# Optimization experiments

Hardware: AMD Instinct MI355X
Metric: run time of the kernel (lower is better)

## Reference

```python
import jax, jax.numpy as jnp
import numpy as np

B, S, D, H = 4, 2048, 1024, 16
HD = D // H

def setup_inputs() -> dict:
    key = jax.random.key(0)
    ks = jax.random.split(key, 11)
    s = 1.0 / np.sqrt(D)
    return {
        "q": jax.random.normal(ks[0], (B, S, D), jnp.float32),
        "k": jax.random.normal(ks[1], (B, S, D), jnp.float32),
        "v": jax.random.normal(ks[2], (B, S, D), jnp.float32),
        "Wq": jax.random.normal(ks[3], (D, D), jnp.float32) * s,
        "bq": jax.random.normal(ks[4], (D,), jnp.float32) * 0.01,
        "Wk": jax.random.normal(ks[5], (D, D), jnp.float32) * s,
        "bk": jax.random.normal(ks[6], (D,), jnp.float32) * 0.01,
        "Wv": jax.random.normal(ks[7], (D, D), jnp.float32) * s,
        "bv": jax.random.normal(ks[8], (D,), jnp.float32) * 0.01,
        "Wo": jax.random.normal(ks[9], (D, D), jnp.float32) * s,
        "bo": jax.random.normal(ks[10], (D,), jnp.float32) * 0.01,
    }

def reference(q, k, v, Wq, bq, Wk, bk, Wv, bv, Wo, bo):
    # linear projections + ReLU activation (as in the torch module)
    qh = jax.nn.relu(q @ Wq.T + bq)
    kh = jax.nn.relu(k @ Wk.T + bk)
    vh = jax.nn.relu(v @ Wv.T + bv)
    # split heads: [B,S,D] -> [B,H,S,HD]
    def split(x):
        return x.reshape(B, S, H, HD).transpose(0, 2, 1, 3)
    qh, kh, vh = split(qh), split(kh), split(vh)
    scale = 1.0 / np.sqrt(HD).astype(np.float32)
    scores = jnp.einsum("bhqd,bhkd->bhqk", qh, kh) * scale
    attn = jax.nn.softmax(scores, axis=-1)
    y = jnp.einsum("bhqk,bhkd->bhqd", attn, vh)
    # merge heads: [B,H,S,HD] -> [B,S,D]
    y = y.transpose(0, 2, 1, 3).reshape(B, S, D)
    return jax.nn.relu(y @ Wo.T + bo)
```

## Files before the change

### kernel.cpp

```cpp
#include <hip/hip_runtime.h>
#include <hip/hip_bf16.h>
#include <cstdint>
#include <cstddef>

#define Bc 4
#define Sc 2048
#define Dc 1024
#define Hc 16

typedef __bf16 bf16;
typedef bf16  bf16x4 __attribute__((ext_vector_type(4)));
typedef bf16  bf16x8 __attribute__((ext_vector_type(8)));
typedef float f32x4  __attribute__((ext_vector_type(4)));

__device__ __forceinline__ void load_lds16(const bf16* g, bf16* l) {
    __builtin_amdgcn_global_load_lds((const __attribute__((address_space(1))) void*)g,
                                     (__attribute__((address_space(3))) void*)l,
                                     16, 0, 0);
}

__device__ __forceinline__ void cvt16(const float* __restrict__ g,
                                      bf16x8& lo, bf16x8& hi) {
    const f32x4 a0 = *(const f32x4*)(g);
    const f32x4 a1 = *(const f32x4*)(g + 4);
    const f32x4 a2 = *(const f32x4*)(g + 8);
    const f32x4 a3 = *(const f32x4*)(g + 12);
#pragma unroll
    for (int j = 0; j < 4; j++) {
        lo[j]     = (bf16)a0[j];
        lo[j + 4] = (bf16)a1[j];
        hi[j]     = (bf16)a2[j];
        hi[j + 4] = (bf16)a3[j];
    }
}

__device__ __forceinline__ void store_relu(float* p, float v) { *p = fmaxf(v, 0.0f); }
__device__ __forceinline__ void store_relu(bf16*  p, float v) { *p = (bf16)fmaxf(v, 0.0f); }

__global__ __launch_bounds__(256)
void cvt_f32_bf16(const float* __restrict__ src, bf16* __restrict__ dst, int n16) {
    const int idx = blockIdx.x * 256 + threadIdx.x;
    if (idx >= n16) return;
    bf16x8 lo, hi;
    cvt16(src + (size_t)idx * 16, lo, hi);
    *(bf16x8*)(dst + (size_t)idx * 16)     = lo;
    *(bf16x8*)(dst + (size_t)idx * 16 + 8) = hi;
}

__global__ __launch_bounds__(256)
void cvt_w4(const float* __restrict__ s0, const float* __restrict__ s1,
            const float* __restrict__ s2, const float* __restrict__ s3,
            bf16* __restrict__ dst) {
    const float* srcs[4] = {s0, s1, s2, s3};
    const float* src = srcs[blockIdx.y];
    const int idx = blockIdx.x * 256 + threadIdx.x;
    bf16x8 lo, hi;
    cvt16(src + (size_t)idx * 16, lo, hi);
    bf16* d = dst + (size_t)blockIdx.y * ((size_t)Dc * Dc) + (size_t)idx * 16;
    *(bf16x8*)d       = lo;
    *(bf16x8*)(d + 8) = hi;
}

#define BM 128
#define BN 64
#define BK 64

template <typename TC, bool TR>
__global__ __launch_bounds__(256)
void gemm_bb(const bf16* __restrict__ A, const bf16* __restrict__ W,
             const float* __restrict__ bias, TC* __restrict__ C,
             int M, int N, int K) {
    __shared__ __align__(16) char pool[24576];
    bf16* lA = (bf16*)pool;
    bf16* lB = (bf16*)(pool + 16384);

    const int t    = threadIdx.x;
    const int lane = t & 63;
    const int wave = t >> 6;
    const int l15  = lane & 15;
    const int quad = lane >> 4;

    const int m0 = blockIdx.x * BM;
    const int n0 = blockIdx.y * BN;
    const int wm = (wave >> 1) * 64;
    const int wn = (wave & 1) * 32;

    f32x4 acc[4][2] = {};

    const int srow = t >> 3;
    const int cg   = (((t & 7) ^ (srow & 7)) << 3);
    const bf16* gA = A + (size_t)(m0 + srow) * K + cg;
    const bf16* gW = W + (size_t)(n0 + srow) * K + cg;
    bf16* lA0 = lA + t * 8;
    bf16* lB0 = lB + t * 8;

    for (int k0 = 0; k0 < K; k0 += BK) {
        __syncthreads();
#pragma unroll
        for (int c = 0; c < 4; c++)
            load_lds16(gA + (size_t)(32 * c) * K, lA0 + c * 2048);
#pragma unroll
        for (int c = 0; c < 2; c++)
            load_lds16(gW + (size_t)(32 * c) * K, lB0 + c * 2048);
        gA += BK; gW += BK;
        __syncthreads();

#pragma unroll
        for (int ks = 0; ks < 2; ks++) {
            bf16x8 af[4], bfr[2];
            const int colp = ((((ks << 2) | quad) ^ (l15 & 7)) << 3);
#pragma unroll
            for (int mt = 0; mt < 4; mt++) {
                const int row = wm + mt * 16 + l15;
                af[mt] = *(const bf16x8*)(lA + row * BK + colp);
            }
#pragma unroll
            for (int nt = 0; nt < 2; nt++) {
                const int row = wn + nt * 16 + l15;
                bfr[nt] = *(const bf16x8*)(lB + row * BK + colp);
            }
#pragma unroll
            for (int mt = 0; mt < 4; mt++)
#pragma unroll
                for (int nt = 0; nt < 2; nt++)
                    acc[mt][nt] = __builtin_amdgcn_mfma_f32_16x16x32_bf16(
                        af[mt], bfr[nt], acc[mt][nt], 0, 0, 0);
        }
    }

    if constexpr (!TR) {
#pragma unroll
        for (int nt = 0; nt < 2; nt++) {
            const int col = n0 + wn + nt * 16 + l15;
            const float bv = bias[col];
#pragma unroll
            for (int mt = 0; mt < 4; mt++) {
                const int rowb = m0 + wm + mt * 16 + quad * 4;
#pragma unroll
                for (int i = 0; i < 4; i++)
                    store_relu(&C[(size_t)(rowb + i) * N + col], acc[mt][nt][i] + bv);
            }
        }
    } else {
        __syncthreads();
        bf16* trp = (bf16*)pool;
#pragma unroll
        for (int nt = 0; nt < 2; nt++) {
            const int col = n0 + wn + nt * 16 + l15;
            const float bv = bias[col];
#pragma unroll
            for (int mt = 0; mt < 4; mt++)
#pragma unroll
                for (int i = 0; i < 4; i++)
                    trp[((wave * 32) + nt * 16 + l15) * 72 + mt * 16 + quad * 4 + i] =
                        (bf16)fmaxf(acc[mt][nt][i] + bv, 0.0f);
        }
        __syncthreads();
        const int r2 = lane >> 3;
        const int c8 = (lane & 7) * 8;
#pragma unroll
        for (int rr = 0; rr < 4; rr++) {
            const int rt = rr * 8 + r2;
            const bf16x8 vv = *(const bf16x8*)&trp[((wave * 32) + rt) * 72 + c8];
            const int cg2 = n0 + wn + rt;
            const int h   = cg2 >> 6, hd = cg2 & 63;
            const int mg  = m0 + wm + c8;
            const int b   = mg >> 11, s = mg & (Sc - 1);
            bf16* dst = (bf16*)C + ((size_t)(b * Hc + h) * 64 + hd) * Sc + s;
            *(bf16x8*)dst = vv;
        }
    }
}

#define QI 4

__global__ __launch_bounds__(256)
void attn_flash(const bf16* __restrict__ Qh, const bf16* __restrict__ Kh,
                const bf16* __restrict__ Vt_g, bf16* __restrict__ Y) {
    __shared__ __align__(16) bf16 Kl[64][64];
    __shared__ __align__(16) bf16 Vl[64][64];
    __shared__ __align__(16) bf16 Pl[4][64][64];

    const int t    = threadIdx.x;
    const int lane = t & 63;
    const int wave = t >> 6;
    const int l15  = lane & 15;
    const int quad = lane >> 4;
    const int rswz = (l15 & 7) * 8;

    const int bh = blockIdx.x;
    const int qt = blockIdx.y;
    const int b  = bh >> 4;
    const int h  = bh & 15;
    const int q0 = qt * 256;
    const size_t rowbase = (size_t)b * Sc;
    const size_t vhead   = (size_t)(b * Hc + h) * 64;

    const float qscale = 0.125f * 1.44269504f;
    bf16x8 qf[QI][2];
#pragma unroll
    for (int qi = 0; qi < QI; qi++) {
        const bf16* qp = Qh + (rowbase + q0 + wave * 64 + qi * 16 + l15) * (size_t)Dc + h * 64;
#pragma unroll
        for (int ks = 0; ks < 2; ks++) {
            const bf16x8 raw = *(const bf16x8*)(qp + ks * 32 + quad * 8);
#pragma unroll
            for (int j = 0; j < 8; j++) qf[qi][ks][j] = (bf16)((float)raw[j] * qscale);
        }
    }

    bf16x8 ones;
#pragma unroll
    for (int j = 0; j < 8; j++) ones[j] = (bf16)1.0f;

    f32x4 yacc[QI][4] = {};
    f32x4 sacc[QI]    = {};

    const int sr = t >> 2;
    const int sc = (t & 3) * 16;
    const int wswz = (sr & 7) * 8;
    const int sc0 = sc ^ wswz;
    const int sc1 = (sc + 8) ^ wswz;
    constexpr int NT = Sc / 64;

    const bf16* kp = Kh + (rowbase + sr) * (size_t)Dc + h * 64 + sc;
    const bf16* vp = Vt_g + (vhead + sr) * (size_t)Sc + sc;
    bf16x8 k0 = *(const bf16x8*)kp;
    bf16x8 k1 = *(const bf16x8*)(kp + 8);
    bf16x8 v0 = *(const bf16x8*)vp;
    bf16x8 v1 = *(const bf16x8*)(vp + 8);

    for (int kt = 0; kt < NT; kt++) {
        __syncthreads();
        *(bf16x8*)&Kl[sr][sc0] = k0;
        *(bf16x8*)&Kl[sr][sc1] = k1;
        *(bf16x8*)&Vl[sr][sc0] = v0;
        *(bf16x8*)&Vl[sr][sc1] = v1;
        __syncthreads();

        if (kt + 1 < NT) {
            kp += (size_t)64 * Dc;
            vp += 64;
            k0 = *(const bf16x8*)kp;
            k1 = *(const bf16x8*)(kp + 8);
            v0 = *(const bf16x8*)vp;
            v1 = *(const bf16x8*)(vp + 8);
        }

        bf16x8 kf[4][2];
#pragma unroll
        for (int mt = 0; mt < 4; mt++) {
            kf[mt][0] = *(const bf16x8*)&Kl[mt * 16 + l15][(quad * 8) ^ rswz];
            kf[mt][1] = *(const bf16x8*)&Kl[mt * 16 + l15][(32 + quad * 8) ^ rswz];
        }

#pragma unroll
        for (int qi = 0; qi < QI; qi++) {
            f32x4 s[4];
            __builtin_amdgcn_s_setprio(1);
#pragma unroll
            for (int mt = 0; mt < 4; mt++) {
                s[mt] = (f32x4){0.f, 0.f, 0.f, 0.f};
                s[mt] = __builtin_amdgcn_mfma_f32_16x16x32_bf16(
                    kf[mt][0], qf[qi][0], s[mt], 0, 0, 0);
                s[mt] = __builtin_amdgcn_mfma_f32_16x16x32_bf16(
                    kf[mt][1], qf[qi][1], s[mt], 0, 0, 0);
            }
            __builtin_amdgcn_s_setprio(0);
#pragma unroll
            for (int mt = 0; mt < 4; mt++) {
                bf16x4 pk;
#pragma unroll
                for (int i = 0; i < 4; i++)
                    pk[i] = (bf16)__builtin_amdgcn_exp2f(s[mt][i]);
                *(bf16x4*)&Pl[wave][qi * 16 + l15][(mt * 16 + quad * 4) ^ rswz] = pk;
            }
        }

        bf16x8 vf[4][2];
#pragma unroll
        for (int nt = 0; nt < 4; nt++) {
            vf[nt][0] = *(const bf16x8*)&Vl[nt * 16 + l15][(quad * 8) ^ rswz];
            vf[nt][1] = *(const bf16x8*)&Vl[nt * 16 + l15][(32 + quad * 8) ^ rswz];
        }

        bf16x8 pf[QI][2];
#pragma unroll
        for (int qi = 0; qi < QI; qi++) {
            pf[qi][0] = *(const bf16x8*)&Pl[wave][qi * 16 + l15][(quad * 8) ^ rswz];
            pf[qi][1] = *(const bf16x8*)&Pl[wave][qi * 16 + l15][(32 + quad * 8) ^ rswz];
        }
        __builtin_amdgcn_s_setprio(1);
#pragma unroll
        for (int qi = 0; qi < QI; qi++) {
            sacc[qi] = __builtin_amdgcn_mfma_f32_16x16x32_bf16(ones, pf[qi][0], sacc[qi], 0, 0, 0);
            sacc[qi] = __builtin_amdgcn_mfma_f32_16x16x32_bf16(ones, pf[qi][1], sacc[qi], 0, 0, 0);
#pragma unroll
            for (int nt = 0; nt < 4; nt++) {
                yacc[qi][nt] = __builtin_amdgcn_mfma_f32_16x16x32_bf16(
                    vf[nt][0], pf[qi][0], yacc[qi][nt], 0, 0, 0);
                yacc[qi][nt] = __builtin_amdgcn_mfma_f32_16x16x32_bf16(
                    vf[nt][1], pf[qi][1], yacc[qi][nt], 0, 0, 0);
            }
        }
        __builtin_amdgcn_s_setprio(0);
    }

#pragma unroll
    for (int qi = 0; qi < QI; qi++) {
        const float inv = 1.0f / sacc[qi][0];
        bf16* yp = Y + (rowbase + q0 + wave * 64 + qi * 16 + l15) * (size_t)Dc + h * 64;
#pragma unroll
        for (int nt = 0; nt < 4; nt++)
#pragma unroll
            for (int i = 0; i < 4; i++)
                yp[nt * 16 + quad * 4 + i] = (bf16)(yacc[qi][nt][i] * inv);
    }
}

extern "C" void kernel_launch(void* const* d_in, const int* in_sizes, int n_in,
                              void* d_out, int out_size, void* d_ws, size_t ws_size,
                              hipStream_t stream) {
    const float* q  = (const float*)d_in[0];
    const float* k  = (const float*)d_in[1];
    const float* v  = (const float*)d_in[2];
    const float* Wq = (const float*)d_in[3];
    const float* bq = (const float*)d_in[4];
    const float* Wk = (const float*)d_in[5];
    const float* bk = (const float*)d_in[6];
    const float* Wv = (const float*)d_in[7];
    const float* bv = (const float*)d_in[8];
    const float* Wo = (const float*)d_in[9];
    const float* bo = (const float*)d_in[10];
    float* out = (float*)d_out;

    const int M = Bc * Sc;
    const int N = Dc;
    const int K = Dc;
    const size_t E  = (size_t)Bc * Sc * Dc;
    const size_t EW = (size_t)Dc * Dc;

    bf16* Qh   = (bf16*)d_out;
    bf16* Kh   = Qh + E;
    bf16* tmpA = (bf16*)d_ws;
    bf16* VtG  = tmpA + E;
    bf16* Wqb  = VtG + E;
    bf16* Wkb  = Wqb + EW;
    bf16* Wvb  = Wkb + EW;
    bf16* Wob  = Wvb + EW;

    const int n16  = (int)(E / 16);
    const int n16w = (int)(EW / 16);
    dim3 gc(n16 / 256);
    dim3 gw4(n16w / 256, 4);
    dim3 gg(M / BM, N / BN);
    dim3 ga(Bc * Hc, Sc / 256);

    cvt_w4<<<gw4, 256, 0, stream>>>(Wq, Wk, Wv, Wo, Wqb);

    cvt_f32_bf16<<<gc, 256, 0, stream>>>(q, tmpA, n16);
    gemm_bb<bf16, false><<<gg, 256, 0, stream>>>(tmpA, Wqb, bq, Qh, M, N, K);

    cvt_f32_bf16<<<gc, 256, 0, stream>>>(k, tmpA, n16);
    gemm_bb<bf16, false><<<gg, 256, 0, stream>>>(tmpA, Wkb, bk, Kh, M, N, K);

    cvt_f32_bf16<<<gc, 256, 0, stream>>>(v, tmpA, n16);
    gemm_bb<bf16, true><<<gg, 256, 0, stream>>>(tmpA, Wvb, bv, VtG, M, N, K);

    attn_flash<<<ga, 256, 0, stream>>>(Qh, Kh, VtG, tmpA);

    gemm_bb<float, false><<<gg, 256, 0, stream>>>(tmpA, Wob, bo, out, M, N, K);
}
```

Measured before the change: 382.2 us.

## Load K/V fragments directly from global into registers with double buffering

Removes the shared-memory staging of K and V tiles and the two block barriers per tile. Each wave now loads its MFMA operand fragments straight from global memory, using two register sets so the next tile's loads overlap the current tile's compute. Launch bounds now request two blocks per CU. The cost is that every wave fetches the full K/V tile itself (four times the global/L2 traffic per block), the fragment reads are uncoalesced 16-byte accesses, and register pressure rises under the occupancy cap.

```diff
diff --git a/kernel.cpp b/kernel.cpp
--- a/kernel.cpp
+++ b/kernel.cpp
@@ -174,11 +174,9 @@
 
 #define QI 4
 
-__global__ __launch_bounds__(256)
+__global__ __launch_bounds__(256, 2)
 void attn_flash(const bf16* __restrict__ Qh, const bf16* __restrict__ Kh,
                 const bf16* __restrict__ Vt_g, bf16* __restrict__ Y) {
-    __shared__ __align__(16) bf16 Kl[64][64];
-    __shared__ __align__(16) bf16 Vl[64][64];
     __shared__ __align__(16) bf16 Pl[4][64][64];
 
     const int t    = threadIdx.x;
@@ -216,44 +214,21 @@
     f32x4 yacc[QI][4] = {};
     f32x4 sacc[QI]    = {};
 
-    const int sr = t >> 2;
-    const int sc = (t & 3) * 16;
-    const int wswz = (sr & 7) * 8;
-    const int sc0 = sc ^ wswz;
-    const int sc1 = (sc + 8) ^ wswz;
-    constexpr int NT = Sc / 64;
-
-    const bf16* kp = Kh + (rowbase + sr) * (size_t)Dc + h * 64 + sc;
-    const bf16* vp = Vt_g + (vhead + sr) * (size_t)Sc + sc;
-    bf16x8 k0 = *(const bf16x8*)kp;
-    bf16x8 k1 = *(const bf16x8*)(kp + 8);
-    bf16x8 v0 = *(const bf16x8*)vp;
-    bf16x8 v1 = *(const bf16x8*)(vp + 8);
-
-    for (int kt = 0; kt < NT; kt++) {
-        __syncthreads();
-        *(bf16x8*)&Kl[sr][sc0] = k0;
-        *(bf16x8*)&Kl[sr][sc1] = k1;
-        *(bf16x8*)&Vl[sr][sc0] = v0;
-        *(bf16x8*)&Vl[sr][sc1] = v1;
-        __syncthreads();
-
-        if (kt + 1 < NT) {
-            kp += (size_t)64 * Dc;
-            vp += 64;
-            k0 = *(const bf16x8*)kp;
-            k1 = *(const bf16x8*)(kp + 8);
-            v0 = *(const bf16x8*)vp;
-            v1 = *(const bf16x8*)(vp + 8);
-        }
-
-        bf16x8 kf[4][2];
+    const bf16* kbase = Kh   + (rowbase + l15) * (size_t)Dc + h * 64 + quad * 8;
+    const bf16* vbase = Vt_g + (vhead   + l15) * (size_t)Sc + quad * 8;
+
+    auto load_tile = [&](bf16x8 (&kd)[4][2], bf16x8 (&vd)[4][2], int kb) {
 #pragma unroll
         for (int mt = 0; mt < 4; mt++) {
-            kf[mt][0] = *(const bf16x8*)&Kl[mt * 16 + l15][(quad * 8) ^ rswz];
-            kf[mt][1] = *(const bf16x8*)&Kl[mt * 16 + l15][(32 + quad * 8) ^ rswz];
-        }
-
+#pragma unroll
+            for (int ks = 0; ks < 2; ks++) {
+                kd[mt][ks] = *(const bf16x8*)(kbase + (size_t)(kb + mt * 16) * Dc + ks * 32);
+                vd[mt][ks] = *(const bf16x8*)(vbase + (size_t)(mt * 16) * Sc + kb + ks * 32);
+            }
+        }
+    };
+
+    auto compute_tile = [&](const bf16x8 (&kc)[4][2], const bf16x8 (&vc)[4][2]) {
 #pragma unroll
         for (int qi = 0; qi < QI; qi++) {
             f32x4 s[4];
@@ -262,9 +237,9 @@
             for (int mt = 0; mt < 4; mt++) {
                 s[mt] = (f32x4){0.f, 0.f, 0.f, 0.f};
                 s[mt] = __builtin_amdgcn_mfma_f32_16x16x32_bf16(
-                    kf[mt][0], qf[qi][0], s[mt], 0, 0, 0);
+                    kc[mt][0], qf[qi][0], s[mt], 0, 0, 0);
                 s[mt] = __builtin_amdgcn_mfma_f32_16x16x32_bf16(
-                    kf[mt][1], qf[qi][1], s[mt], 0, 0, 0);
+                    kc[mt][1], qf[qi][1], s[mt], 0, 0, 0);
             }
             __builtin_amdgcn_s_setprio(0);
 #pragma unroll
@@ -277,13 +252,6 @@
             }
         }
 
-        bf16x8 vf[4][2];
-#pragma unroll
-        for (int nt = 0; nt < 4; nt++) {
-            vf[nt][0] = *(const bf16x8*)&Vl[nt * 16 + l15][(quad * 8) ^ rswz];
-            vf[nt][1] = *(const bf16x8*)&Vl[nt * 16 + l15][(32 + quad * 8) ^ rswz];
-        }
-
         bf16x8 pf[QI][2];
 #pragma unroll
         for (int qi = 0; qi < QI; qi++) {
@@ -298,12 +266,24 @@
 #pragma unroll
             for (int nt = 0; nt < 4; nt++) {
                 yacc[qi][nt] = __builtin_amdgcn_mfma_f32_16x16x32_bf16(
-                    vf[nt][0], pf[qi][0], yacc[qi][nt], 0, 0, 0);
+                    vc[nt][0], pf[qi][0], yacc[qi][nt], 0, 0, 0);
                 yacc[qi][nt] = __builtin_amdgcn_mfma_f32_16x16x32_bf16(
-                    vf[nt][1], pf[qi][1], yacc[qi][nt], 0, 0, 0);
+                    vc[nt][1], pf[qi][1], yacc[qi][nt], 0, 0, 0);
             }
         }
         __builtin_amdgcn_s_setprio(0);
+    };
+
+    constexpr int NT = Sc / 64;
+    bf16x8 kA[4][2], vA[4][2], kB[4][2], vB[4][2];
+    load_tile(kA, vA, 0);
+#pragma unroll 1
+    for (int kt = 0; kt < NT; kt += 2) {
+        load_tile(kB, vB, (kt + 1) * 64);
+        compute_tile(kA, vA);
+        if (kt + 2 < NT)
+            load_tile(kA, vA, (kt + 2) * 64);
+        compute_tile(kB, vB);
     }
 
 #pragma unroll
```

Result: slower. 484.3 us (+26.7%).
